# Performance work log

Measured on AMD Instinct MI355X. Metric: run time of the kernel, lower is better.

Reference implementation:

```python
import jax, jax.numpy as jnp
import numpy as np

TOP_K = 8


def setup_inputs() -> dict:
    key = jax.random.key(0)
    ks = jax.random.split(key, 5)
    B, S, H, E, I = 2, 1024, 2048, 64, 768
    return {
        "hidden_states": jax.random.normal(ks[0], (B, S, H), dtype=jnp.float32),
        "router_w": jax.random.normal(ks[1], (H, E), dtype=jnp.float32) * 0.02,
        "gate_w": jax.random.normal(ks[2], (E, H, I), dtype=jnp.float32) * 0.02,
        "up_w": jax.random.normal(ks[3], (E, H, I), dtype=jnp.float32) * 0.02,
        "down_w": jax.random.normal(ks[4], (E, I, H), dtype=jnp.float32) * 0.02,
    }


def reference(hidden_states, router_w, gate_w, up_w, down_w):
    B, S, H = hidden_states.shape
    E = router_w.shape[1]
    x = hidden_states.reshape(-1, H)                      # [T, H]
    T = x.shape[0]

    router_logits = x @ router_w                           # [T, E]
    probs = jax.nn.softmax(router_logits.astype(jnp.float32), axis=-1)
    topk_w, topk_idx = jax.lax.top_k(probs, TOP_K)         # [T, K]
    topk_w = topk_w / jnp.sum(topk_w, axis=-1, keepdims=True)  # norm_topk_prob
    topk_w = topk_w.astype(x.dtype)

    # Dense combine weights: zero for non-selected experts -> same math as the
    # gather/scatter loop, jit-friendly (no data-dependent shapes).
    combine = jnp.zeros((T, E), dtype=x.dtype)
    combine = combine.at[jnp.arange(T)[:, None], topk_idx].set(topk_w)  # [T, E]

    g = jnp.einsum('th,ehi->tei', x, gate_w)               # [T, E, I]
    u = jnp.einsum('th,ehi->tei', x, up_w)                 # [T, E, I]
    h = jax.nn.silu(g) * u                                 # SwiGLU
    out = jnp.einsum('te,tei,eih->th', combine, h, down_w)  # weighted combine

    return out.reshape(B, S, H), router_logits
```

## Files before the change

kernel.cpp:

```cpp
#include <hip/hip_runtime.h>
#include <hip/hip_bf16.h>

typedef __hip_bfloat16 bf16;
typedef short s16x8 __attribute__((ext_vector_type(8)));
typedef unsigned short u16x8 __attribute__((ext_vector_type(8)));
typedef float f32x4 __attribute__((ext_vector_type(4)));

#define T_TOK 2048
#define HDIM  2048
#define NEXP  64
#define IDIM  768
#define TOPK  8
#define OUT_OFF (T_TOK * HDIM)
#define NPAIR (T_TOK * TOPK)

#define WS_TOPK_IDX  0
#define WS_TOPK_W    (64 * 1024)
#define WS_PAIR_TOK  (128 * 1024)
#define WS_SLOT_OF   (192 * 1024)
#define WS_COUNTS    (256 * 1024)
#define WS_OFFSETS   (257 * 1024)
#define WS_CURSOR    (258 * 1024)
#define WS_H         (1024 * 1024)
#define WS_PARTIAL   (WS_H + (size_t)NPAIR * IDIM * 2)
#define WS_XB        WS_PARTIAL

__device__ __forceinline__ float bf_to_f(unsigned short u) {
    return __uint_as_float(((unsigned int)u) << 16);
}
__device__ __forceinline__ unsigned short f2bf(float f) {
    unsigned int u = __float_as_uint(f);
    unsigned int r = (u + 0x7FFFu + ((u >> 16) & 1u)) >> 16;
    return (unsigned short)r;
}
__device__ __forceinline__ unsigned cvtpk(float lo, float hi) {
    unsigned r;
    asm("v_cvt_pk_bf16_f32 %0, %1, %2" : "=v"(r) : "v"(lo), "v"(hi));
    return r;
}

typedef const __attribute__((address_space(1))) unsigned int* gas_ptr;
typedef __attribute__((address_space(3))) unsigned int* las_ptr;
__device__ __forceinline__ void gload_lds16(const void* g, void* l) {
    __builtin_amdgcn_global_load_lds((gas_ptr)g, (las_ptr)l, 16, 0, 0);
}

__global__ __launch_bounds__(256) void xbf_kernel(const float* __restrict__ x,
                                                  unsigned short* __restrict__ xb) {
    int i = blockIdx.x * 256 + threadIdx.x;
    const float4* src = (const float4*)x + (size_t)i * 2;
    float4 a = src[0], b = src[1];
    u16x8 o;
    o[0] = f2bf(a.x); o[1] = f2bf(a.y); o[2] = f2bf(a.z); o[3] = f2bf(a.w);
    o[4] = f2bf(b.x); o[5] = f2bf(b.y); o[6] = f2bf(b.z); o[7] = f2bf(b.w);
    ((u16x8*)xb)[i] = o;
}

__global__ __launch_bounds__(256) void router_kernel(
    const float* __restrict__ x, const float* __restrict__ rw,
    float* __restrict__ logits) {
    int wave = threadIdx.x >> 6;
    int lane = threadIdx.x & 63;
    int t = blockIdx.x * 4 + wave;
    const float4* x4 = (const float4*)(x + (size_t)t * HDIM);
    float acc = 0.f;
    for (int h4 = 0; h4 < HDIM / 4; ++h4) {
        float4 xv = x4[h4];
        int h = h4 * 4;
        acc = fmaf(xv.x, rw[(h + 0) * NEXP + lane], acc);
        acc = fmaf(xv.y, rw[(h + 1) * NEXP + lane], acc);
        acc = fmaf(xv.z, rw[(h + 2) * NEXP + lane], acc);
        acc = fmaf(xv.w, rw[(h + 3) * NEXP + lane], acc);
    }
    logits[t * NEXP + lane] = acc;
}

__global__ __launch_bounds__(64) void topk_kernel(
    const float* __restrict__ logits, int* __restrict__ topk_idx,
    float* __restrict__ topk_w, int* __restrict__ counts) {
    int t = blockIdx.x;
    int lane = threadIdx.x;
    float lg = logits[t * NEXP + lane];
    float mx = lg;
    for (int off = 32; off; off >>= 1) mx = fmaxf(mx, __shfl_xor(mx, off));
    float ex = expf(lg - mx);
    float sum = ex;
    for (int off = 32; off; off >>= 1) sum += __shfl_xor(sum, off);
    float prob = ex / sum;

    float pr = prob;
    float myv = 0.f;
    int myidx = 0;
    float ksum = 0.f;
    for (int k = 0; k < TOPK; ++k) {
        float v = pr;
        int idx = lane;
        for (int off = 32; off; off >>= 1) {
            float ov = __shfl_xor(v, off);
            int oi = __shfl_xor(idx, off);
            if (ov > v || (ov == v && oi < idx)) { v = ov; idx = oi; }
        }
        ksum += v;
        if (lane == k) { myidx = idx; myv = v; }
        if (lane == idx) pr = -1.f;
    }
    if (lane < TOPK) {
        topk_idx[t * TOPK + lane] = myidx;
        topk_w[t * TOPK + lane] = myv / ksum;
        atomicAdd(&counts[myidx], 1);
    }
}

__global__ __launch_bounds__(64) void scan_kernel(
    const int* __restrict__ counts, int* __restrict__ offsets, int* __restrict__ cursor) {
    int lane = threadIdx.x;
    int c = counts[lane];
    int incl = c;
    for (int off = 1; off < 64; off <<= 1) {
        int tt = __shfl_up(incl, off);
        if (lane >= off) incl += tt;
    }
    offsets[lane] = incl - c;
    if (lane == 63) offsets[64] = incl;
    cursor[lane] = 0;
}

__global__ __launch_bounds__(256) void scatter_kernel(
    const int* __restrict__ topk_idx, const int* __restrict__ offsets,
    int* __restrict__ cursor, int* __restrict__ pair_token, int* __restrict__ slot_of) {
    int i = blockIdx.x * 256 + threadIdx.x;
    if (i >= NPAIR) return;
    int t = i >> 3;
    int e = topk_idx[i];
    int pos = atomicAdd(&cursor[e], 1);
    int slot = offsets[e] + pos;
    pair_token[slot] = t;
    slot_of[i] = slot;
}

#define BM   256
#define BKS  32
#define BROW 40
#define NKG  (HDIM / BKS)
#define NKD  (IDIM / BKS)

__global__ __launch_bounds__(512, 4) void gateup_mfma(
    const unsigned short* __restrict__ xb, const float* __restrict__ gate_w,
    const float* __restrict__ up_w, const int* __restrict__ offsets,
    const int* __restrict__ pair_token, unsigned short* __restrict__ hbuf) {
    int id = blockIdx.x;
    int b = id & 7, rid = id >> 3;
    int ntile = rid % 12;
    int e = b + 8 * (rid / 12);
    int off = offsets[e];
    int cnt = offsets[e + 1] - off;
    if (cnt <= 0) return;

    __shared__ unsigned short As[2][BM * BKS];
    __shared__ unsigned short Bgu[2][128 * BROW];
    __shared__ int toks[BM];

    int tid = threadIdx.x;
    int lane = tid & 63;
    int wave = tid >> 6;
    int wr = wave >> 1, wc = wave & 1;
    int l15 = lane & 15, lg4 = lane >> 4;

    int mat = tid >> 8;
    int rem = tid & 255;
    int nI2 = rem & 31, kc8 = rem >> 5;
    int brow = mat * 64 + nI2 * 2;
    int bslot = (kc8 ^ (nI2 & 7)) * 4;
    const float* bsrc = (mat ? up_w : gate_w) + (size_t)e * HDIM * IDIM
                        + (size_t)(kc8 * 4) * IDIM + ntile * 64 + nI2 * 2;

    int arowq = tid >> 2;
    int ac = tid & 3;

    for (int mt = 0; mt * BM < cnt; ++mt) {
        int m0 = mt * BM;
        if (tid < BM) {
            int p = m0 + tid;
            toks[tid] = pair_token[off + (p < cnt ? p : cnt - 1)];
        }
        __syncthreads();
        const unsigned short* aq[2];
        #pragma unroll
        for (int q = 0; q < 2; ++q) {
            int row = q * 128 + arowq;
            int j2 = ac ^ (row & 3) ^ ((row >> 2) & 3);
            aq[q] = xb + (size_t)toks[row] * HDIM + j2 * 8;
        }
        f32x4 accg[4][2] = {};
        f32x4 accu[4][2] = {};

        gload_lds16(aq[0], &As[0][tid * 8]);
        gload_lds16(aq[1], &As[0][(512 + tid) * 8]);
        float2 Bv[4];
        #pragma unroll
        for (int i = 0; i < 4; ++i)
            Bv[i] = *(const float2*)(bsrc + (size_t)i * IDIM);

        for (int ks = 0; ks < NKG; ++ks) {
            int p = ks & 1;
            {
                uint2 w0, w1;
                w0.x = cvtpk(Bv[0].x, Bv[1].x); w0.y = cvtpk(Bv[2].x, Bv[3].x);
                w1.x = cvtpk(Bv[0].y, Bv[1].y); w1.y = cvtpk(Bv[2].y, Bv[3].y);
                *(uint2*)&Bgu[p][brow * BROW + bslot] = w0;
                *(uint2*)&Bgu[p][(brow + 1) * BROW + bslot] = w1;
            }
            __syncthreads();
            if (ks + 1 < NKG) {
                int h1 = (ks + 1) * BKS;
                gload_lds16(aq[0] + h1, &As[p ^ 1][tid * 8]);
                gload_lds16(aq[1] + h1, &As[p ^ 1][(512 + tid) * 8]);
                #pragma unroll
                for (int i = 0; i < 4; ++i)
                    Bv[i] = *(const float2*)(bsrc + (size_t)((ks + 1) * BKS + i) * IDIM);
            }
            s16x8 a[4];
            #pragma unroll
            for (int mr = 0; mr < 4; ++mr) {
                int r = wr * 64 + mr * 16 + l15;
                int sa = lg4 ^ (r & 3) ^ ((r >> 2) & 3);
                a[mr] = *(const s16x8*)&As[p][r * BKS + sa * 8];
            }
            #pragma unroll
            for (int nr = 0; nr < 2; ++nr) {
                int ng = wc * 32 + nr * 16 + l15;
                int s0 = ((2 * lg4) ^ ((ng >> 1) & 7)) * 4;
                int s1 = ((2 * lg4 + 1) ^ ((ng >> 1) & 7)) * 4;
                s16x8 bg, bu;
                *(uint2*)&bg = *(const uint2*)&Bgu[p][ng * BROW + s0];
                *((uint2*)&bg + 1) = *(const uint2*)&Bgu[p][ng * BROW + s1];
                *(uint2*)&bu = *(const uint2*)&Bgu[p][(64 + ng) * BROW + s0];
                *((uint2*)&bu + 1) = *(const uint2*)&Bgu[p][(64 + ng) * BROW + s1];
                #pragma unroll
                for (int mr = 0; mr < 4; ++mr) {
                    accg[mr][nr] = __builtin_amdgcn_mfma_f32_16x16x32_bf16(a[mr], bg, accg[mr][nr], 0, 0, 0);
                    accu[mr][nr] = __builtin_amdgcn_mfma_f32_16x16x32_bf16(a[mr], bu, accu[mr][nr], 0, 0, 0);
                }
            }
        }

        #pragma unroll
        for (int mr = 0; mr < 4; ++mr)
            #pragma unroll
            for (int nr = 0; nr < 2; ++nr) {
                int col = ntile * 64 + wc * 32 + nr * 16 + l15;
                #pragma unroll
                for (int reg = 0; reg < 4; ++reg) {
                    int r = m0 + wr * 64 + mr * 16 + lg4 * 4 + reg;
                    if (r < cnt) {
                        float g = accg[mr][nr][reg];
                        float u = accu[mr][nr][reg];
                        float hv = (g / (1.f + __expf(-g))) * u;
                        hbuf[(size_t)(off + r) * IDIM + col] = f2bf(hv);
                    }
                }
            }
        __syncthreads();
    }
}

__global__ __launch_bounds__(512, 4) void down_mfma(
    const unsigned short* __restrict__ hbuf, const float* __restrict__ down_w,
    const int* __restrict__ offsets, unsigned short* __restrict__ partial) {
    int id = blockIdx.x;
    int b = id & 7, rid = id >> 3;
    int ntile = rid % 16;
    int e = b + 8 * (rid / 16);
    int off = offsets[e];
    int cnt = offsets[e + 1] - off;
    if (cnt <= 0) return;

    __shared__ unsigned short As[2][BM * BKS];
    __shared__ unsigned short Bd[2][128 * BROW];

    int tid = threadIdx.x;
    int lane = tid & 63;
    int wave = tid >> 6;
    int wr = wave >> 1, wc = wave & 1;
    int l15 = lane & 15, lg4 = lane >> 4;

    int nI2 = tid & 63, kc8 = tid >> 6;
    int brow = nI2 * 2;
    int bslot = (kc8 ^ (nI2 & 7)) * 4;
    const float* bsrc = down_w + (size_t)e * IDIM * HDIM
                        + (size_t)(kc8 * 4) * HDIM + ntile * 128 + nI2 * 2;

    int arowq = tid >> 2;
    int ac = tid & 3;

    for (int mt = 0; mt * BM < cnt; ++mt) {
        int m0 = mt * BM;
        __syncthreads();
        const unsigned short* aq[2];
        #pragma unroll
        for (int q = 0; q < 2; ++q) {
            int row = q * 128 + arowq;
            int rr = m0 + row;
            if (rr >= cnt) rr = cnt - 1;
            int j2 = ac ^ (row & 3) ^ ((row >> 2) & 3);
            aq[q] = hbuf + (size_t)(off + rr) * IDIM + j2 * 8;
        }
        f32x4 acc[4][4] = {};

        gload_lds16(aq[0], &As[0][tid * 8]);
        gload_lds16(aq[1], &As[0][(512 + tid) * 8]);
        float2 Bv[4];
        #pragma unroll
        for (int i = 0; i < 4; ++i)
            Bv[i] = *(const float2*)(bsrc + (size_t)i * HDIM);

        for (int ks = 0; ks < NKD; ++ks) {
            int p = ks & 1;
            {
                uint2 w0, w1;
                w0.x = cvtpk(Bv[0].x, Bv[1].x); w0.y = cvtpk(Bv[2].x, Bv[3].x);
                w1.x = cvtpk(Bv[0].y, Bv[1].y); w1.y = cvtpk(Bv[2].y, Bv[3].y);
                *(uint2*)&Bd[p][brow * BROW + bslot] = w0;
                *(uint2*)&Bd[p][(brow + 1) * BROW + bslot] = w1;
            }
            __syncthreads();
            if (ks + 1 < NKD) {
                int k1 = (ks + 1) * BKS;
                gload_lds16(aq[0] + k1, &As[p ^ 1][tid * 8]);
                gload_lds16(aq[1] + k1, &As[p ^ 1][(512 + tid) * 8]);
                #pragma unroll
                for (int i = 0; i < 4; ++i)
                    Bv[i] = *(const float2*)(bsrc + (size_t)(k1 + i) * HDIM);
            }
            s16x8 a[4];
            #pragma unroll
            for (int mr = 0; mr < 4; ++mr) {
                int r = wr * 64 + mr * 16 + l15;
                int sa = lg4 ^ (r & 3) ^ ((r >> 2) & 3);
                a[mr] = *(const s16x8*)&As[p][r * BKS + sa * 8];
            }
            #pragma unroll
            for (int nr = 0; nr < 4; ++nr) {
                int n = wc * 64 + nr * 16 + l15;
                int s0 = ((2 * lg4) ^ ((n >> 1) & 7)) * 4;
                int s1 = ((2 * lg4 + 1) ^ ((n >> 1) & 7)) * 4;
                s16x8 bb;
                *(uint2*)&bb = *(const uint2*)&Bd[p][n * BROW + s0];
                *((uint2*)&bb + 1) = *(const uint2*)&Bd[p][n * BROW + s1];
                #pragma unroll
                for (int mr = 0; mr < 4; ++mr)
                    acc[mr][nr] = __builtin_amdgcn_mfma_f32_16x16x32_bf16(a[mr], bb, acc[mr][nr], 0, 0, 0);
            }
        }

        #pragma unroll
        for (int mr = 0; mr < 4; ++mr)
            #pragma unroll
            for (int nr = 0; nr < 4; ++nr) {
                int col = ntile * 128 + wc * 64 + nr * 16 + l15;
                #pragma unroll
                for (int reg = 0; reg < 4; ++reg) {
                    int r = m0 + wr * 64 + mr * 16 + lg4 * 4 + reg;
                    if (r < cnt)
                        partial[(size_t)(off + r) * HDIM + col] = f2bf(acc[mr][nr][reg]);
                }
            }
        __syncthreads();
    }
}

__global__ __launch_bounds__(256) void reduce_kernel(
    const unsigned short* __restrict__ partial, const int* __restrict__ slot_of,
    const float* __restrict__ topk_w, float* __restrict__ out) {
    int t = blockIdx.x;
    int j8 = threadIdx.x * 8;
    __shared__ int ss[8];
    __shared__ float sw[8];
    if (threadIdx.x < 8) {
        ss[threadIdx.x] = slot_of[t * TOPK + threadIdx.x];
        sw[threadIdx.x] = topk_w[t * TOPK + threadIdx.x];
    }
    __syncthreads();
    float acc[8] = {};
    #pragma unroll
    for (int k = 0; k < TOPK; ++k) {
        u16x8 v = *(const u16x8*)&partial[(size_t)ss[k] * HDIM + j8];
        float w = sw[k];
        #pragma unroll
        for (int i = 0; i < 8; ++i)
            acc[i] = fmaf(w, bf_to_f((unsigned short)v[i]), acc[i]);
    }
    float4 o0 = {acc[0], acc[1], acc[2], acc[3]};
    float4 o1 = {acc[4], acc[5], acc[6], acc[7]};
    *(float4*)&out[(size_t)t * HDIM + j8] = o0;
    *(float4*)&out[(size_t)t * HDIM + j8 + 4] = o1;
}

extern "C" void kernel_launch(void* const* d_in, const int* in_sizes, int n_in,
                              void* d_out, int out_size, void* d_ws, size_t ws_size,
                              hipStream_t stream) {
    const float* x  = (const float*)d_in[0];
    const float* rw = (const float*)d_in[1];
    const float* gw = (const float*)d_in[2];
    const float* uw = (const float*)d_in[3];
    const float* dw = (const float*)d_in[4];
    float* out = (float*)d_out;
    float* logits = out + OUT_OFF;

    char* ws = (char*)d_ws;
    int*   topk_idx   = (int*)(ws + WS_TOPK_IDX);
    float* topk_w     = (float*)(ws + WS_TOPK_W);
    int*   pair_token = (int*)(ws + WS_PAIR_TOK);
    int*   slot_of    = (int*)(ws + WS_SLOT_OF);
    int*   counts     = (int*)(ws + WS_COUNTS);
    int*   offsets    = (int*)(ws + WS_OFFSETS);
    int*   cursor     = (int*)(ws + WS_CURSOR);
    unsigned short* hbuf    = (unsigned short*)(ws + WS_H);
    unsigned short* partial = (unsigned short*)(ws + WS_PARTIAL);
    unsigned short* xb      = (unsigned short*)(ws + WS_XB);

    hipMemsetAsync(counts, 0, NEXP * sizeof(int), stream);
    xbf_kernel<<<T_TOK * HDIM / (256 * 8), 256, 0, stream>>>(x, xb);
    router_kernel<<<T_TOK / 4, 256, 0, stream>>>(x, rw, logits);
    topk_kernel<<<T_TOK, 64, 0, stream>>>(logits, topk_idx, topk_w, counts);
    scan_kernel<<<1, 64, 0, stream>>>(counts, offsets, cursor);
    scatter_kernel<<<NPAIR / 256, 256, 0, stream>>>(topk_idx, offsets, cursor, pair_token, slot_of);
    gateup_mfma<<<NEXP * 12, 512, 0, stream>>>(xb, gw, uw, offsets, pair_token, hbuf);
    down_mfma<<<NEXP * 16, 512, 0, stream>>>(hbuf, dw, offsets, partial);
    reduce_kernel<<<dim3(T_TOK, 1), 256, 0, stream>>>(partial, slot_of, topk_w, out);
}
```

Measured before the change: 714.2 us.

## Use chunk-major unswizzled LDS layouts with wide 16-byte fragment reads

```diff
diff --git a/kernel.cpp b/kernel.cpp
--- a/kernel.cpp
+++ b/kernel.cpp
@@ -156,9 +156,8 @@
     int cnt = offsets[e + 1] - off;
     if (cnt <= 0) return;
 
-    __shared__ unsigned short As[2][BM * BKS];
+    __shared__ unsigned short As[2][1024 * 8];
     __shared__ unsigned short Bgu[2][128 * BROW];
-    __shared__ int toks[BM];
 
     int tid = threadIdx.x;
     int lane = tid & 63;
@@ -168,34 +167,27 @@
 
     int mat = tid >> 8;
     int rem = tid & 255;
-    int nI2 = rem & 31, kc8 = rem >> 5;
-    int brow = mat * 64 + nI2 * 2;
-    int bslot = (kc8 ^ (nI2 & 7)) * 4;
+    int kc = rem & 7, nI2 = rem >> 3;
+    int browB = mat * 64 + nI2 * 2;
+    int bslot = kc * 4;
     const float* bsrc = (mat ? up_w : gate_w) + (size_t)e * HDIM * IDIM
-                        + (size_t)(kc8 * 4) * IDIM + ntile * 64 + nI2 * 2;
-
-    int arowq = tid >> 2;
-    int ac = tid & 3;
+                        + (size_t)(kc * 4) * IDIM + ntile * 64 + nI2 * 2;
+
+    int am = tid & 255;
+    int jj0 = tid >> 8;
 
     for (int mt = 0; mt * BM < cnt; ++mt) {
         int m0 = mt * BM;
-        if (tid < BM) {
-            int p = m0 + tid;
-            toks[tid] = pair_token[off + (p < cnt ? p : cnt - 1)];
-        }
+        int prow = m0 + am;
+        int tk = pair_token[off + (prow < cnt ? prow : cnt - 1)];
+        const unsigned short* asrc = xb + (size_t)tk * HDIM + jj0 * 8;
         __syncthreads();
-        const unsigned short* aq[2];
-        #pragma unroll
-        for (int q = 0; q < 2; ++q) {
-            int row = q * 128 + arowq;
-            int j2 = ac ^ (row & 3) ^ ((row >> 2) & 3);
-            aq[q] = xb + (size_t)toks[row] * HDIM + j2 * 8;
-        }
+
         f32x4 accg[4][2] = {};
         f32x4 accu[4][2] = {};
 
-        gload_lds16(aq[0], &As[0][tid * 8]);
-        gload_lds16(aq[1], &As[0][(512 + tid) * 8]);
+        gload_lds16(asrc, &As[0][tid * 8]);
+        gload_lds16(asrc + 16, &As[0][(512 + tid) * 8]);
         float2 Bv[4];
         #pragma unroll
         for (int i = 0; i < 4; ++i)
@@ -207,35 +199,29 @@
                 uint2 w0, w1;
                 w0.x = cvtpk(Bv[0].x, Bv[1].x); w0.y = cvtpk(Bv[2].x, Bv[3].x);
                 w1.x = cvtpk(Bv[0].y, Bv[1].y); w1.y = cvtpk(Bv[2].y, Bv[3].y);
-                *(uint2*)&Bgu[p][brow * BROW + bslot] = w0;
-                *(uint2*)&Bgu[p][(brow + 1) * BROW + bslot] = w1;
+                *(uint2*)&Bgu[p][browB * BROW + bslot] = w0;
+                *(uint2*)&Bgu[p][(browB + 1) * BROW + bslot] = w1;
             }
             __syncthreads();
             if (ks + 1 < NKG) {
                 int h1 = (ks + 1) * BKS;
-                gload_lds16(aq[0] + h1, &As[p ^ 1][tid * 8]);
-                gload_lds16(aq[1] + h1, &As[p ^ 1][(512 + tid) * 8]);
+                gload_lds16(asrc + h1, &As[p ^ 1][tid * 8]);
+                gload_lds16(asrc + h1 + 16, &As[p ^ 1][(512 + tid) * 8]);
                 #pragma unroll
                 for (int i = 0; i < 4; ++i)
-                    Bv[i] = *(const float2*)(bsrc + (size_t)((ks + 1) * BKS + i) * IDIM);
+                    Bv[i] = *(const float2*)(bsrc + (size_t)(h1 + i) * IDIM);
             }
             s16x8 a[4];
             #pragma unroll
             for (int mr = 0; mr < 4; ++mr) {
                 int r = wr * 64 + mr * 16 + l15;
-                int sa = lg4 ^ (r & 3) ^ ((r >> 2) & 3);
-                a[mr] = *(const s16x8*)&As[p][r * BKS + sa * 8];
+                a[mr] = *(const s16x8*)&As[p][(lg4 * 256 + r) * 8];
             }
             #pragma unroll
             for (int nr = 0; nr < 2; ++nr) {
                 int ng = wc * 32 + nr * 16 + l15;
-                int s0 = ((2 * lg4) ^ ((ng >> 1) & 7)) * 4;
-                int s1 = ((2 * lg4 + 1) ^ ((ng >> 1) & 7)) * 4;
-                s16x8 bg, bu;
-                *(uint2*)&bg = *(const uint2*)&Bgu[p][ng * BROW + s0];
-                *((uint2*)&bg + 1) = *(const uint2*)&Bgu[p][ng * BROW + s1];
-                *(uint2*)&bu = *(const uint2*)&Bgu[p][(64 + ng) * BROW + s0];
-                *((uint2*)&bu + 1) = *(const uint2*)&Bgu[p][(64 + ng) * BROW + s1];
+                s16x8 bg = *(const s16x8*)&Bgu[p][ng * BROW + lg4 * 8];
+                s16x8 bu = *(const s16x8*)&Bgu[p][(64 + ng) * BROW + lg4 * 8];
                 #pragma unroll
                 for (int mr = 0; mr < 4; ++mr) {
                     accg[mr][nr] = __builtin_amdgcn_mfma_f32_16x16x32_bf16(a[mr], bg, accg[mr][nr], 0, 0, 0);
@@ -275,7 +261,7 @@
     int cnt = offsets[e + 1] - off;
     if (cnt <= 0) return;
 
-    __shared__ unsigned short As[2][BM * BKS];
+    __shared__ unsigned short As[2][1024 * 8];
     __shared__ unsigned short Bd[2][128 * BROW];
 
     int tid = threadIdx.x;
@@ -284,31 +270,26 @@
     int wr = wave >> 1, wc = wave & 1;
     int l15 = lane & 15, lg4 = lane >> 4;
 
-    int nI2 = tid & 63, kc8 = tid >> 6;
-    int brow = nI2 * 2;
-    int bslot = (kc8 ^ (nI2 & 7)) * 4;
+    int kc = tid & 7, nI2 = tid >> 3;
+    int browB = nI2 * 2;
+    int bslot = kc * 4;
     const float* bsrc = down_w + (size_t)e * IDIM * HDIM
-                        + (size_t)(kc8 * 4) * HDIM + ntile * 128 + nI2 * 2;
-
-    int arowq = tid >> 2;
-    int ac = tid & 3;
+                        + (size_t)(kc * 4) * HDIM + ntile * 128 + nI2 * 2;
+
+    int am = tid & 255;
+    int jj0 = tid >> 8;
 
     for (int mt = 0; mt * BM < cnt; ++mt) {
         int m0 = mt * BM;
+        int prow = m0 + am;
+        if (prow >= cnt) prow = cnt - 1;
+        const unsigned short* asrc = hbuf + (size_t)(off + prow) * IDIM + jj0 * 8;
         __syncthreads();
-        const unsigned short* aq[2];
-        #pragma unroll
-        for (int q = 0; q < 2; ++q) {
-            int row = q * 128 + arowq;
-            int rr = m0 + row;
-            if (rr >= cnt) rr = cnt - 1;
-            int j2 = ac ^ (row & 3) ^ ((row >> 2) & 3);
-            aq[q] = hbuf + (size_t)(off + rr) * IDIM + j2 * 8;
-        }
+
         f32x4 acc[4][4] = {};
 
-        gload_lds16(aq[0], &As[0][tid * 8]);
-        gload_lds16(aq[1], &As[0][(512 + tid) * 8]);
+        gload_lds16(asrc, &As[0][tid * 8]);
+        gload_lds16(asrc + 16, &As[0][(512 + tid) * 8]);
         float2 Bv[4];
         #pragma unroll
         for (int i = 0; i < 4; ++i)
@@ -320,14 +301,14 @@
                 uint2 w0, w1;
                 w0.x = cvtpk(Bv[0].x, Bv[1].x); w0.y = cvtpk(Bv[2].x, Bv[3].x);
                 w1.x = cvtpk(Bv[0].y, Bv[1].y); w1.y = cvtpk(Bv[2].y, Bv[3].y);
-                *(uint2*)&Bd[p][brow * BROW + bslot] = w0;
-                *(uint2*)&Bd[p][(brow + 1) * BROW + bslot] = w1;
+                *(uint2*)&Bd[p][browB * BROW + bslot] = w0;
+                *(uint2*)&Bd[p][(browB + 1) * BROW + bslot] = w1;
             }
             __syncthreads();
             if (ks + 1 < NKD) {
                 int k1 = (ks + 1) * BKS;
-                gload_lds16(aq[0] + k1, &As[p ^ 1][tid * 8]);
-                gload_lds16(aq[1] + k1, &As[p ^ 1][(512 + tid) * 8]);
+                gload_lds16(asrc + k1, &As[p ^ 1][tid * 8]);
+                gload_lds16(asrc + k1 + 16, &As[p ^ 1][(512 + tid) * 8]);
                 #pragma unroll
                 for (int i = 0; i < 4; ++i)
                     Bv[i] = *(const float2*)(bsrc + (size_t)(k1 + i) * HDIM);
@@ -336,21 +317,19 @@
             #pragma unroll
             for (int mr = 0; mr < 4; ++mr) {
                 int r = wr * 64 + mr * 16 + l15;
-                int sa = lg4 ^ (r & 3) ^ ((r >> 2) & 3);
-                a[mr] = *(const s16x8*)&As[p][r * BKS + sa * 8];
-            }
+                a[mr] = *(const s16x8*)&As[p][(lg4 * 256 + r) * 8];
+            }
+            s16x8 bb[4];
             #pragma unroll
             for (int nr = 0; nr < 4; ++nr) {
                 int n = wc * 64 + nr * 16 + l15;
-                int s0 = ((2 * lg4) ^ ((n >> 1) & 7)) * 4;
-                int s1 = ((2 * lg4 + 1) ^ ((n >> 1) & 7)) * 4;
-                s16x8 bb;
-                *(uint2*)&bb = *(const uint2*)&Bd[p][n * BROW + s0];
-                *((uint2*)&bb + 1) = *(const uint2*)&Bd[p][n * BROW + s1];
-                #pragma unroll
-                for (int mr = 0; mr < 4; ++mr)
-                    acc[mr][nr] = __builtin_amdgcn_mfma_f32_16x16x32_bf16(a[mr], bb, acc[mr][nr], 0, 0, 0);
-            }
+                bb[nr] = *(const s16x8*)&Bd[p][n * BROW + lg4 * 8];
+            }
+            #pragma unroll
+            for (int mr = 0; mr < 4; ++mr)
+                #pragma unroll
+                for (int nr = 0; nr < 4; ++nr)
+                    acc[mr][nr] = __builtin_amdgcn_mfma_f32_16x16x32_bf16(a[mr], bb[nr], acc[mr][nr], 0, 0, 0);
         }
 
         #pragma unroll
```

After: 1.037 ms. 45.2% more time.
